# Kernel tuning notes

Hardware: AMD Instinct MI355X
Metric: run time of the kernel (lower is better)

The kernel has to match this reference:

```python
import jax, jax.numpy as jnp
import numpy as np

N_NODES = 200_000
N_EDGES = 6_400_000
N_GRAPHS = 512


def _graph_conv(x, src, dst, W_rel, b_rel, W_root, n_nodes):
    # PyG GraphConv (aggr='add'): lin_rel(sum_{j->i} x_j) + lin_root(x_i)
    agg = jax.ops.segment_sum(x[src], dst, num_segments=n_nodes)  # [N, in]
    return agg @ W_rel.T + b_rel + x @ W_root.T


def setup_inputs() -> dict:
    key = jax.random.key(0)
    ks = jax.random.split(key, 12)
    x = jax.random.normal(ks[0], (N_NODES, 3), dtype=jnp.float32)
    edge_index = jax.random.randint(ks[1], (2, N_EDGES), 0, N_NODES, dtype=jnp.int64)
    batch = jnp.sort(jax.random.randint(ks[2], (N_NODES,), 0, N_GRAPHS, dtype=jnp.int64))

    def xavier(k, shape):
        fan_out, fan_in = shape
        lim = np.sqrt(6.0 / (fan_in + fan_out)).astype(np.float32)
        return jax.random.uniform(k, shape, jnp.float32, -lim, lim)

    return {
        "x": x, "edge_index": edge_index, "batch": batch,
        "W1_rel": xavier(ks[3], (32, 3)),  "b1": jnp.zeros((32,), jnp.float32), "W1_root": xavier(ks[4], (32, 3)),
        "W2_rel": xavier(ks[5], (16, 32)), "b2": jnp.zeros((16,), jnp.float32), "W2_root": xavier(ks[6], (16, 32)),
        "W3_rel": xavier(ks[7], (8, 16)),  "b3": jnp.zeros((8,), jnp.float32),  "W3_root": xavier(ks[8], (8, 16)),
        "W_lin": xavier(ks[9], (1, 8)),    "b_lin": jnp.zeros((1,), jnp.float32),
    }


def reference(x, edge_index, batch,
              W1_rel, b1, W1_root,
              W2_rel, b2, W2_root,
              W3_rel, b3, W3_root,
              W_lin, b_lin):
    src, dst = edge_index[0], edge_index[1]
    h = jax.nn.relu(_graph_conv(x, src, dst, W1_rel, b1, W1_root, N_NODES))
    h = jax.nn.relu(_graph_conv(h, src, dst, W2_rel, b2, W2_root, N_NODES))
    h = jax.nn.relu(_graph_conv(h, src, dst, W3_rel, b3, W3_root, N_NODES))
    pooled = jax.ops.segment_max(h, batch, num_segments=N_GRAPHS)  # [G, 8]
    out = pooled @ W_lin.T + b_lin  # [G, 1]
    return out[:, 0]
```

## Files before the change

### kernel.cpp

```cpp
#include <hip/hip_runtime.h>
#include <hip/hip_fp16.h>

#define N_NODES 200000
#define N_EDGES 6400000
#define N_GRAPHS 512
#define HALFN 100000

#define NB1 196
#define CB 1024
#define NSB 16
#define NFB (NB1 * NSB)
#define CHUNK 4096
#define NCH 1563
#define NGRP 25
#define CPG 63
#define SCAP 3072
#define NBLK32 (N_NODES / 32)

typedef float vf4 __attribute__((ext_vector_type(4)));
typedef float vf2 __attribute__((ext_vector_type(2)));
typedef unsigned vu2 __attribute__((ext_vector_type(2)));

__device__ __forceinline__ unsigned ntload_u(const unsigned* p) {
  return __builtin_nontemporal_load(p);
}
__device__ __forceinline__ int ntload_i(const int* p) { return __builtin_nontemporal_load(p); }
__device__ __forceinline__ float ntload_f(const float* p) {
  return __builtin_nontemporal_load(p);
}
__device__ __forceinline__ void ntstore_u(unsigned* p, unsigned v) {
  __builtin_nontemporal_store(v, p);
}

__global__ __launch_bounds__(256) void count_kernel(const int* __restrict__ dst,
                                                    unsigned short* __restrict__ H) {
  __shared__ unsigned hist[4][NB1];
  int t = threadIdx.x, w = t >> 6;
  for (int i = t; i < 4 * NB1; i += 256) ((unsigned*)hist)[i] = 0;
  __syncthreads();
  int c = blockIdx.x;
  long e0 = (long)c * CHUNK;
  long rem = (long)N_EDGES - e0;
  int n = rem > CHUNK ? CHUNK : (int)rem;
  for (int i = t; i < n; i += 256) atomicAdd(&hist[w][dst[e0 + i] >> 10], 1u);
  __syncthreads();
  for (int b = t; b < NB1; b += 256)
    H[(size_t)c * NB1 + b] =
        (unsigned short)(hist[0][b] + hist[1][b] + hist[2][b] + hist[3][b]);
}

__global__ __launch_bounds__(256) void scan_bins1_kernel(unsigned short* __restrict__ H,
                                                         unsigned* __restrict__ P) {
  int b = blockIdx.x * 256 + threadIdx.x;
  int g = blockIdx.y;
  if (b >= NB1) return;
  int c0 = g * CPG, c1 = min(NCH, (g + 1) * CPG);
  unsigned run = 0;
  for (int c = c0; c < c1; c++) {
    unsigned t = H[(size_t)c * NB1 + b];
    H[(size_t)c * NB1 + b] = (unsigned short)run;
    run += t;
  }
  P[(size_t)g * NB1 + b] = run;
}

__global__ __launch_bounds__(256) void scan_bins2_kernel(unsigned* __restrict__ P,
                                                         unsigned* __restrict__ bucketTotal) {
  int b = blockIdx.x * 256 + threadIdx.x;
  if (b >= NB1) return;
  unsigned run = 0;
  for (int g = 0; g < NGRP; g++) {
    unsigned t = P[(size_t)g * NB1 + b];
    P[(size_t)g * NB1 + b] = run;
    run += t;
  }
  bucketTotal[b] = run;
}

__global__ __launch_bounds__(256) void scan_total_kernel(const unsigned* __restrict__ bucketTotal,
                                                         unsigned* __restrict__ bucketStart) {
  __shared__ unsigned partial[256];
  int t = threadIdx.x;
  unsigned v = (t < NB1) ? bucketTotal[t] : 0u;
  partial[t] = v;
  __syncthreads();
  for (int off = 1; off < 256; off <<= 1) {
    unsigned add = (t >= off) ? partial[t - off] : 0u;
    __syncthreads();
    partial[t] += add;
    __syncthreads();
  }
  if (t < NB1) bucketStart[t] = partial[t] - v;
  if (t == 0) bucketStart[NB1] = N_EDGES;
}

__global__ __launch_bounds__(256) void scatterA_kernel(
    const int* __restrict__ src, const int* __restrict__ dst,
    const unsigned short* __restrict__ H, const unsigned* __restrict__ P,
    const unsigned* __restrict__ bucketStart, unsigned* __restrict__ X1) {
  __shared__ unsigned ssort[CHUNK];
  __shared__ unsigned char sbort[CHUNK];
  __shared__ unsigned histw[4][NB1];
  __shared__ unsigned curw[4][NB1];
  __shared__ unsigned gbase[NB1];
  __shared__ unsigned partial[256];
  int t = threadIdx.x, w = t >> 6;
  int c = blockIdx.x;
  int g = c / CPG;
  long e0 = (long)c * CHUNK;
  long rem = (long)N_EDGES - e0;
  int n = rem > CHUNK ? CHUNK : (int)rem;
  for (int i = t; i < 4 * NB1; i += 256) ((unsigned*)histw)[i] = 0;
  __syncthreads();
  for (int i = t; i < n; i += 256) atomicAdd(&histw[w][dst[e0 + i] >> 10], 1u);
  __syncthreads();
  unsigned tot = 0, h0 = 0, h1 = 0, h2 = 0, h3 = 0;
  if (t < NB1) {
    h0 = histw[0][t]; h1 = histw[1][t]; h2 = histw[2][t]; h3 = histw[3][t];
    tot = h0 + h1 + h2 + h3;
  }
  partial[t] = tot;
  __syncthreads();
  for (int off = 1; off < 256; off <<= 1) {
    unsigned add = (t >= off) ? partial[t - off] : 0u;
    __syncthreads();
    partial[t] += add;
    __syncthreads();
  }
  if (t < NB1) {
    unsigned ex = partial[t] - tot;
    unsigned r = ex;
    curw[0][t] = r; r += h0;
    curw[1][t] = r; r += h1;
    curw[2][t] = r; r += h2;
    curw[3][t] = r;
    gbase[t] = bucketStart[t] + P[(size_t)g * NB1 + t] + (unsigned)H[(size_t)c * NB1 + t] - ex;
  }
  __syncthreads();
  for (int i = t; i < n; i += 256) {
    int d = dst[e0 + i], s = src[e0 + i];
    int b = d >> 10;
    unsigned r = atomicAdd(&curw[w][b], 1u);
    ssort[r] = ((unsigned)s << 10) | (unsigned)(d & 1023);
    sbort[r] = (unsigned char)b;
  }
  __syncthreads();
  for (int j = t; j < n; j += 256) X1[gbase[sbort[j]] + j] = ssort[j];
}

__global__ __launch_bounds__(1024) void scatterB_kernel(
    const unsigned* __restrict__ X1, const unsigned* __restrict__ bucketStart,
    unsigned* __restrict__ X2, unsigned* __restrict__ fineStart) {
  __shared__ unsigned histw[16][NSB];
  __shared__ unsigned binstart[NSB + 1];
  __shared__ unsigned cur[NSB];
  int t = threadIdx.x, w = t >> 6, b = blockIdx.x;
  unsigned cs0 = bucketStart[b], cs1 = bucketStart[b + 1];
  int n = (int)(cs1 - cs0);
  if (t < 16 * NSB) ((unsigned*)histw)[t] = 0;
  __syncthreads();
  for (int i = t; i < n; i += 1024)
    atomicAdd(&histw[w][(X1[cs0 + i] >> 6) & 15u], 1u);
  __syncthreads();
  if (t == 0) {
    unsigned run = 0;
    for (int k = 0; k < NSB; k++) {
      binstart[k] = run;
      unsigned tot = 0;
      for (int ww = 0; ww < 16; ww++) tot += histw[ww][k];
      run += tot;
    }
    binstart[NSB] = run;
  }
  __syncthreads();
  if (t < NSB) {
    fineStart[b * NSB + t] = cs0 + binstart[t];
    cur[t] = binstart[t];
  }
  if (b == NB1 - 1 && t == 0) fineStart[NFB] = cs1;
  __syncthreads();
  for (int i = t; i < n; i += 1024) {
    unsigned v = X1[cs0 + i];
    unsigned pos = atomicAdd(&cur[(v >> 6) & 15u], 1u);
    X2[cs0 + pos] = v;
  }
}

__global__ __launch_bounds__(256) void sort2_kernel(const unsigned* __restrict__ X2,
                                                    const unsigned* __restrict__ fineStart,
                                                    unsigned* __restrict__ packedB,
                                                    unsigned* __restrict__ nodeStart,
                                                    unsigned char* __restrict__ deltaSplit) {
  __shared__ unsigned buf[SCAP];
  __shared__ unsigned buf2[SCAP];
  __shared__ unsigned hist[128], base[128], cur[128];
  int t = threadIdx.x, b = blockIdx.x;
  unsigned s0 = fineStart[b], s1 = fineStart[b + 1];
  int n = (int)(s1 - s0);
  if (t < 128) hist[t] = 0;
  for (int i = t; i < n; i += 256) buf[i] = ntload_u(&X2[s0 + i]);
  __syncthreads();
  for (int i = t; i < n; i += 256) {
    unsigned v = buf[i];
    unsigned bin = ((v & 63u) << 1) | ((v >> 10) >= HALFN ? 1u : 0u);
    atomicAdd(&hist[bin], 1u);
  }
  __syncthreads();
  if (t == 0) {
    unsigned run = 0;
    for (int k = 0; k < 128; k++) {
      unsigned v = hist[k];
      base[k] = run;
      cur[k] = run;
      run += v;
    }
  }
  __syncthreads();
  if (t < 64) {
    int gn = b * 64 + t;
    if (gn <= N_NODES) nodeStart[gn] = s0 + base[2 * t];
    if (gn < N_NODES) deltaSplit[gn] = (unsigned char)(base[2 * t + 1] - base[2 * t]);
  }
  for (int i = t; i < n; i += 256) {
    unsigned v = buf[i];
    unsigned bin = ((v & 63u) << 1) | ((v >> 10) >= HALFN ? 1u : 0u);
    unsigned pos = atomicAdd(&cur[bin], 1u);
    buf2[pos] = v >> 10;
  }
  __syncthreads();
  for (int i = t; i < n; i += 256) ntstore_u(&packedB[s0 + i], buf2[i]);
}

__global__ __launch_bounds__(256) void xpad_kernel(const float* __restrict__ x,
                                                   uint2* __restrict__ xph) {
  int n = blockIdx.x * 256 + threadIdx.x;
  if (n >= N_NODES) return;
  __half2 a = __floats2half2_rn(x[3 * n], x[3 * n + 1]);
  __half2 b = __floats2half2_rn(x[3 * n + 2], 0.f);
  xph[n] = make_uint2(*(unsigned*)&a, *(unsigned*)&b);
}

__device__ __forceinline__ void half8_unpack(uint4 g, float* f) {
  const __half2* h2 = reinterpret_cast<const __half2*>(&g);
#pragma unroll
  for (int j = 0; j < 4; j++) {
    float2 fj = __half22float2(h2[j]);
    f[2 * j] = fj.x;
    f[2 * j + 1] = fj.y;
  }
}

__global__ __launch_bounds__(256) void layer1a_kernel(
    const unsigned* __restrict__ packed, const unsigned* __restrict__ nodeStart,
    const uint2* __restrict__ xph, float* __restrict__ agg) {
  __shared__ float plds[256 * 9];
  int t = threadIdx.x, ln = t >> 3, p = t & 7;
  int node = blockIdx.x * 32 + ln;
  unsigned s1v = ntload_u(&nodeStart[node + 1]);
  float a0 = 0.f, a1 = 0.f, a2 = 0.f;
  for (unsigned base = ntload_u(&nodeStart[node]) + p; base < s1v; base += 32) {
    unsigned i1 = base + 8, i2 = base + 16, i3 = base + 24;
    unsigned e0 = ntload_u(&packed[base]);
    unsigned e1 = ntload_u(&packed[i1]);
    unsigned e2 = ntload_u(&packed[i2]);
    unsigned e3 = ntload_u(&packed[i3]);
    uint2 g0 = xph[e0], g1 = xph[e1], g2 = xph[e2], g3 = xph[e3];
    float m1 = (i1 < s1v) ? 1.f : 0.f;
    float m2 = (i2 < s1v) ? 1.f : 0.f;
    float m3 = (i3 < s1v) ? 1.f : 0.f;
    float2 xy0 = __half22float2(*(const __half2*)&g0.x);
    float2 zw0 = __half22float2(*(const __half2*)&g0.y);
    float2 xy1 = __half22float2(*(const __half2*)&g1.x);
    float2 zw1 = __half22float2(*(const __half2*)&g1.y);
    float2 xy2 = __half22float2(*(const __half2*)&g2.x);
    float2 zw2 = __half22float2(*(const __half2*)&g2.y);
    float2 xy3 = __half22float2(*(const __half2*)&g3.x);
    float2 zw3 = __half22float2(*(const __half2*)&g3.y);
    a0 += xy0.x + m1 * xy1.x + m2 * xy2.x + m3 * xy3.x;
    a1 += xy0.y + m1 * xy1.y + m2 * xy2.y + m3 * xy3.y;
    a2 += zw0.x + m1 * zw1.x + m2 * zw2.x + m3 * zw3.x;
  }
  plds[t * 9] = a0; plds[t * 9 + 1] = a1; plds[t * 9 + 2] = a2;
  __syncthreads();
  if (p < 4) {
    int q0 = ln * 72 + p;
    float v = 0.f;
    if (p < 3)
      v = plds[q0] + plds[q0 + 9] + plds[q0 + 18] + plds[q0 + 27] +
          plds[q0 + 36] + plds[q0 + 45] + plds[q0 + 54] + plds[q0 + 63];
    agg[(size_t)node * 4 + p] = v;
  }
}

__global__ __launch_bounds__(256) void layer1b_kernel(
    const float* __restrict__ x, const float4* __restrict__ agg,
    const float* __restrict__ W1_rel, const float* __restrict__ b1,
    const float* __restrict__ W1_root,
    const float* __restrict__ W2_rel, const float* __restrict__ W2_root,
    uint4* __restrict__ t2h4, uint4* __restrict__ r2h4) {
  __shared__ float sW1rel[96], sW1root[96], sb1[32], sW2rel[512], sW2root[512];
  for (int i = threadIdx.x; i < 96; i += 256) { sW1rel[i] = W1_rel[i]; sW1root[i] = W1_root[i]; }
  for (int i = threadIdx.x; i < 32; i += 256) sb1[i] = b1[i];
  for (int i = threadIdx.x; i < 512; i += 256) { sW2rel[i] = W2_rel[i]; sW2root[i] = W2_root[i]; }
  __syncthreads();
  int node = blockIdx.x * 256 + threadIdx.x;
  if (node >= N_NODES) return;
  float4 A = agg[node];
  float xv0 = x[3 * node], xv1 = x[3 * node + 1], xv2 = x[3 * node + 2];
  float h[32];
#pragma unroll
  for (int k = 0; k < 32; k++) {
    float v = sW1rel[3 * k] * A.x + sW1rel[3 * k + 1] * A.y + sW1rel[3 * k + 2] * A.z +
              sW1root[3 * k] * xv0 + sW1root[3 * k + 1] * xv1 + sW1root[3 * k + 2] * xv2 +
              sb1[k];
    h[k] = fmaxf(v, 0.f);
  }
  unsigned tp[8];
#pragma unroll
  for (int j = 0; j < 16; j += 2) {
    float t0 = 0.f, t1 = 0.f;
#pragma unroll
    for (int k = 0; k < 32; k++) {
      t0 += sW2rel[32 * j + k] * h[k];
      t1 += sW2rel[32 * (j + 1) + k] * h[k];
    }
    __half2 pk = __halves2half2(__float2half_rn(t0), __float2half_rn(t1));
    tp[j >> 1] = *(unsigned*)&pk;
  }
  t2h4[(size_t)node * 2] = make_uint4(tp[0], tp[1], tp[2], tp[3]);
  t2h4[(size_t)node * 2 + 1] = make_uint4(tp[4], tp[5], tp[6], tp[7]);
  unsigned rp[8];
#pragma unroll
  for (int j = 0; j < 16; j += 2) {
    float r0 = 0.f, r1 = 0.f;
#pragma unroll
    for (int k = 0; k < 32; k++) {
      r0 += sW2root[32 * j + k] * h[k];
      r1 += sW2root[32 * (j + 1) + k] * h[k];
    }
    __half2 pk = __halves2half2(__float2half_rn(r0), __float2half_rn(r1));
    rp[j >> 1] = *(unsigned*)&pk;
  }
  r2h4[(size_t)node * 2] = make_uint4(rp[0], rp[1], rp[2], rp[3]);
  r2h4[(size_t)node * 2 + 1] = make_uint4(rp[4], rp[5], rp[6], rp[7]);
}

__global__ __launch_bounds__(256) void layer2g_kernel(
    const unsigned* __restrict__ packed, const unsigned* __restrict__ nodeStart,
    const unsigned char* __restrict__ deltaSplit,
    const uint4* __restrict__ t2h4, __half* __restrict__ agg2, int pass) {
  __shared__ float plds[256 * 17];
  int t = threadIdx.x, ln = t >> 3, p = t & 7;
  int node = blockIdx.x * 32 + ln;
  unsigned s0n = ntload_u(&nodeStart[node]);
  unsigned s1n = ntload_u(&nodeStart[node + 1]);
  unsigned split = s0n + (unsigned)deltaSplit[node];
  unsigned lo = pass ? split : s0n;
  unsigned hi = pass ? s1n : split;
  float acc[16];
#pragma unroll
  for (int j = 0; j < 16; j++) acc[j] = 0.f;
  for (unsigned base = lo + p; base < hi; base += 16) {
    unsigned i1 = base + 8;
    unsigned e0 = ntload_u(&packed[base]);
    unsigned e1r = ntload_u(&packed[i1]);
    bool in1 = i1 < hi;
    unsigned e1 = in1 ? e1r : e0;
    uint4 g0a = t2h4[(size_t)e0 * 2], g0b = t2h4[(size_t)e0 * 2 + 1];
    uint4 g1a = t2h4[(size_t)e1 * 2], g1b = t2h4[(size_t)e1 * 2 + 1];
    float f0[16], f1[16];
    half8_unpack(g0a, f0);
    half8_unpack(g0b, f0 + 8);
    half8_unpack(g1a, f1);
    half8_unpack(g1b, f1 + 8);
    float m1 = in1 ? 1.f : 0.f;
#pragma unroll
    for (int j = 0; j < 16; j++) acc[j] += f0[j] + m1 * f1[j];
  }
#pragma unroll
  for (int j = 0; j < 16; j++) plds[t * 17 + j] = acc[j];
  __syncthreads();
  int qb = ln * 8 * 17;
  float s0 = 0.f, s1 = 0.f;
#pragma unroll
  for (int k = 0; k < 8; k++) {
    s0 += plds[qb + k * 17 + 2 * p];
    s1 += plds[qb + k * 17 + 2 * p + 1];
  }
  __half* dst = &agg2[(size_t)node * 16 + 2 * p];
  if (pass) {
    __half2 old = *(const __half2*)dst;
    float2 of = __half22float2(old);
    s0 += of.x;
    s1 += of.y;
  }
  *(__half2*)dst = __halves2half2(__float2half_rn(s0), __float2half_rn(s1));
}

__global__ __launch_bounds__(256) void layer2e_kernel(
    const uint4* agg2q, const uint4* __restrict__ r2h4,
    const float* __restrict__ b2, const float* __restrict__ W3_rel,
    const float* __restrict__ W3_root, uint4* __restrict__ t3h4, float4* r34) {
  __shared__ float sW3rel[128], sW3root[128], sb2[16];
  for (int i = threadIdx.x; i < 128; i += 256) { sW3rel[i] = W3_rel[i]; sW3root[i] = W3_root[i]; }
  if (threadIdx.x < 16) sb2[threadIdx.x] = b2[threadIdx.x];
  __syncthreads();
  int node = blockIdx.x * 256 + threadIdx.x;
  if (node >= N_NODES) return;
  uint4 ga = agg2q[(size_t)node * 2];
  uint4 gb = agg2q[(size_t)node * 2 + 1];
  float ag[16];
  half8_unpack(ga, ag);
  half8_unpack(gb, ag + 8);
  uint4 ra = r2h4[(size_t)node * 2];
  uint4 rb = r2h4[(size_t)node * 2 + 1];
  float rv2[16];
  half8_unpack(ra, rv2);
  half8_unpack(rb, rv2 + 8);
  float h[16];
#pragma unroll
  for (int k = 0; k < 16; k++) h[k] = fmaxf(ag[k] + rv2[k] + sb2[k], 0.f);
  unsigned tp[4];
#pragma unroll
  for (int j = 0; j < 8; j += 2) {
    float t0 = 0.f, t1 = 0.f;
#pragma unroll
    for (int k = 0; k < 16; k++) {
      t0 += sW3rel[16 * j + k] * h[k];
      t1 += sW3rel[16 * (j + 1) + k] * h[k];
    }
    __half2 pk = __halves2half2(__float2half_rn(t0), __float2half_rn(t1));
    tp[j >> 1] = *(unsigned*)&pk;
  }
  t3h4[node] = make_uint4(tp[0], tp[1], tp[2], tp[3]);
  float rv[8];
#pragma unroll
  for (int j = 0; j < 8; j++) {
    float a = 0.f;
#pragma unroll
    for (int k = 0; k < 16; k++) a += sW3root[16 * j + k] * h[k];
    rv[j] = a;
  }
  r34[(size_t)node * 2] = make_float4(rv[0], rv[1], rv[2], rv[3]);
  r34[(size_t)node * 2 + 1] = make_float4(rv[4], rv[5], rv[6], rv[7]);
}

__global__ __launch_bounds__(256) void layer3_kernel(
    const unsigned* __restrict__ packed, const unsigned* __restrict__ nodeStart,
    const uint4* __restrict__ t3h4, const float* __restrict__ r3,
    const float* __restrict__ b3,
    const int* __restrict__ batch, unsigned* __restrict__ pooled) {
  __shared__ float plds[256 * 9];
  __shared__ float sb3[8];
  __shared__ int sgid[32];
  if (threadIdx.x < 8) sb3[threadIdx.x] = b3[threadIdx.x];
  __syncthreads();
  int t = threadIdx.x, ln = t >> 3, p = t & 7;
  int node = blockIdx.x * 32 + ln;
  unsigned s1v = ntload_u(&nodeStart[node + 1]);
  float acc[8];
#pragma unroll
  for (int j = 0; j < 8; j++) acc[j] = 0.f;
  for (unsigned base = ntload_u(&nodeStart[node]) + p; base < s1v; base += 32) {
    unsigned i1 = base + 8, i2 = base + 16, i3 = base + 24;
    unsigned e0 = ntload_u(&packed[base]);
    unsigned e1 = ntload_u(&packed[i1]);
    unsigned e2 = ntload_u(&packed[i2]);
    unsigned e3 = ntload_u(&packed[i3]);
    uint4 g0 = t3h4[e0];
    uint4 g1 = t3h4[e1];
    uint4 g2 = t3h4[e2];
    uint4 g3 = t3h4[e3];
    float m1 = (i1 < s1v) ? 1.f : 0.f;
    float m2 = (i2 < s1v) ? 1.f : 0.f;
    float m3 = (i3 < s1v) ? 1.f : 0.f;
    float f0[8], f1[8], f2[8], f3[8];
    half8_unpack(g0, f0);
    half8_unpack(g1, f1);
    half8_unpack(g2, f2);
    half8_unpack(g3, f3);
#pragma unroll
    for (int j = 0; j < 8; j++)
      acc[j] += f0[j] + m1 * f1[j] + m2 * f2[j] + m3 * f3[j];
  }
#pragma unroll
  for (int j = 0; j < 8; j++) plds[t * 9 + j] = acc[j];
  __syncthreads();
  int gg = ntload_i(&batch[node]);
  int q0 = ln * 72 + p;
  float v = plds[q0] + plds[q0 + 9] + plds[q0 + 18] + plds[q0 + 27] +
            plds[q0 + 36] + plds[q0 + 45] + plds[q0 + 54] + plds[q0 + 63];
  float h = fmaxf(v + sb3[p] + ntload_f(&r3[(size_t)node * 8 + p]), 0.f);
  __syncthreads();
  plds[ln * 9 + p] = h;
  if (p == 0) sgid[ln] = gg;
  __syncthreads();
  if (t < 8) {
    int gcur = sgid[0];
    float m = plds[t];
    for (int l = 1; l < 32; l++) {
      int g2 = sgid[l];
      float hv = plds[l * 9 + t];
      if (g2 != gcur) {
        atomicMax(&pooled[8 * gcur + t], __float_as_uint(m));
        gcur = g2;
        m = hv;
      } else {
        m = fmaxf(m, hv);
      }
    }
    atomicMax(&pooled[8 * gcur + t], __float_as_uint(m));
  }
}

__global__ __launch_bounds__(256) void final_kernel(
    const unsigned* __restrict__ pooled, const float* __restrict__ W_lin,
    const float* __restrict__ b_lin, float* __restrict__ out) {
  int g = blockIdx.x * blockDim.x + threadIdx.x;
  if (g >= N_GRAPHS) return;
  float acc = b_lin[0];
#pragma unroll
  for (int f = 0; f < 8; f++) acc += __uint_as_float(pooled[8 * g + f]) * W_lin[f];
  out[g] = acc;
}

extern "C" void kernel_launch(void* const* d_in, const int* in_sizes, int n_in,
                              void* d_out, int out_size, void* d_ws, size_t ws_size,
                              hipStream_t stream) {
  const float* x = (const float*)d_in[0];
  const int* ei = (const int*)d_in[1];
  const int* src = ei;
  const int* dst = ei + N_EDGES;
  const int* batch = (const int*)d_in[2];
  const float* W1_rel = (const float*)d_in[3];
  const float* b1 = (const float*)d_in[4];
  const float* W1_root = (const float*)d_in[5];
  const float* W2_rel = (const float*)d_in[6];
  const float* b2 = (const float*)d_in[7];
  const float* W2_root = (const float*)d_in[8];
  const float* W3_rel = (const float*)d_in[9];
  const float* b3 = (const float*)d_in[10];
  const float* W3_root = (const float*)d_in[11];
  const float* W_lin = (const float*)d_in[12];
  const float* b_lin = (const float*)d_in[13];
  float* out = (float*)d_out;

  char* ws = (char*)d_ws;
  unsigned* X2 = (unsigned*)(ws + 0);
  uint4* r2h = (uint4*)(ws + 0);
  __half* agg2 = (__half*)(ws + 6400000);
  float* r3 = (float*)(ws + 6400000);
  unsigned* t3h = (unsigned*)(ws + 12800000);
  unsigned* t2h = (unsigned*)(ws + 16000000);
  unsigned* X1 = (unsigned*)(ws + 25600000);
  unsigned* packedB = (unsigned*)(ws + 25600000);
  unsigned short* H = (unsigned short*)(ws + 51200128);
  unsigned* P = (unsigned*)(ws + 51812824);
  unsigned* bucketTotal = (unsigned*)(ws + 51832424);
  unsigned* bucketStart = (unsigned*)(ws + 51833208);
  unsigned* fineStart = (unsigned*)(ws + 51833996);
  float* agg = (float*)(ws + 52000000);
  uint2* xpadh = (uint2*)(ws + 55300000);
  unsigned* pooled = (unsigned*)(ws + 57600128);
  unsigned char* deltaSplit = (unsigned char*)(ws + 57616512);
  unsigned* nodeStart = (unsigned*)(ws + 57954016);

  hipMemsetAsync(pooled, 0, N_GRAPHS * 8 * sizeof(unsigned), stream);
  hipMemsetAsync(packedB + N_EDGES, 0, 128, stream);

  xpad_kernel<<<(N_NODES + 255) / 256, 256, 0, stream>>>(x, xpadh);

  count_kernel<<<NCH, 256, 0, stream>>>(dst, H);
  scan_bins1_kernel<<<dim3((NB1 + 255) / 256, NGRP), 256, 0, stream>>>(H, P);
  scan_bins2_kernel<<<(NB1 + 255) / 256, 256, 0, stream>>>(P, bucketTotal);
  scan_total_kernel<<<1, 256, 0, stream>>>(bucketTotal, bucketStart);
  scatterA_kernel<<<NCH, 256, 0, stream>>>(src, dst, H, P, bucketStart, X1);
  scatterB_kernel<<<NB1, 1024, 0, stream>>>(X1, bucketStart, X2, fineStart);
  sort2_kernel<<<NFB, 256, 0, stream>>>(X2, fineStart, packedB, nodeStart, deltaSplit);

  layer1a_kernel<<<NBLK32, 256, 0, stream>>>(packedB, nodeStart, xpadh, agg);
  layer1b_kernel<<<(N_NODES + 255) / 256, 256, 0, stream>>>(
      x, (const float4*)agg, W1_rel, b1, W1_root, W2_rel, W2_root,
      (uint4*)t2h, r2h);

  layer2g_kernel<<<NBLK32, 256, 0, stream>>>(packedB, nodeStart, deltaSplit,
                                             (const uint4*)t2h, agg2, 0);
  layer2g_kernel<<<NBLK32, 256, 0, stream>>>(packedB, nodeStart, deltaSplit,
                                             (const uint4*)t2h, agg2, 1);
  layer2e_kernel<<<(N_NODES + 255) / 256, 256, 0, stream>>>(
      (const uint4*)agg2, (const uint4*)r2h, b2, W3_rel, W3_root,
      (uint4*)t3h, (float4*)r3);

  layer3_kernel<<<NBLK32, 256, 0, stream>>>(packedB, nodeStart, (const uint4*)t3h, r3, b3,
                                            batch, pooled);
  final_kernel<<<(N_GRAPHS + 255) / 256, 256, 0, stream>>>(pooled, W_lin, b_lin, out);
}
```

Before: 416.8 us.

## Fuse second-level scatter and fine sort into one per-bucket LDS sort kernel

Replaces the two-pass scatterB plus sort2 (which wrote an intermediate X2 array to global memory and launched 3136 small blocks) with a single kernel per coarse bucket. Each block builds a 2048-bin histogram of (node, half) keys in shared memory, scans it in parallel, emits nodeStart and deltaSplit, and counting-sorts the bucket's entries into a large LDS buffer before writing packedB. This removes one full global read/write pass over the edge list and a launch. In exchange, only 196 blocks run, with about 150KB of LDS each, so occupancy and parallelism drop and X1 is read twice. Output aliases input memory (X1 and packedB share the same offset), which stays safe only because each block reads its range before storing it.

```diff
diff --git a/kernel.cpp b/kernel.cpp
--- a/kernel.cpp
+++ b/kernel.cpp
@@ -8,13 +8,11 @@
 
 #define NB1 196
 #define CB 1024
-#define NSB 16
-#define NFB (NB1 * NSB)
 #define CHUNK 4096
 #define NCH 1563
 #define NGRP 25
 #define CPG 63
-#define SCAP 3072
+#define BCAP 34816
 #define NBLK32 (N_NODES / 32)
 
 typedef float vf4 __attribute__((ext_vector_type(4)));
@@ -148,87 +146,58 @@
   for (int j = t; j < n; j += 256) X1[gbase[sbort[j]] + j] = ssort[j];
 }
 
-__global__ __launch_bounds__(1024) void scatterB_kernel(
-    const unsigned* __restrict__ X1, const unsigned* __restrict__ bucketStart,
-    unsigned* __restrict__ X2, unsigned* __restrict__ fineStart) {
-  __shared__ unsigned histw[16][NSB];
-  __shared__ unsigned binstart[NSB + 1];
-  __shared__ unsigned cur[NSB];
-  int t = threadIdx.x, w = t >> 6, b = blockIdx.x;
+__global__ __launch_bounds__(512) void sortBC_kernel(
+    const unsigned* X1r, const unsigned* __restrict__ bucketStart,
+    unsigned* packedB, unsigned* __restrict__ nodeStart,
+    unsigned char* __restrict__ deltaSplit) {
+  __shared__ unsigned buf[BCAP];
+  __shared__ unsigned hist[2048];
+  __shared__ unsigned cur[2048];
+  __shared__ unsigned partial[512];
+  int t = threadIdx.x, b = blockIdx.x;
   unsigned cs0 = bucketStart[b], cs1 = bucketStart[b + 1];
   int n = (int)(cs1 - cs0);
-  if (t < 16 * NSB) ((unsigned*)histw)[t] = 0;
-  __syncthreads();
-  for (int i = t; i < n; i += 1024)
-    atomicAdd(&histw[w][(X1[cs0 + i] >> 6) & 15u], 1u);
-  __syncthreads();
-  if (t == 0) {
-    unsigned run = 0;
-    for (int k = 0; k < NSB; k++) {
-      binstart[k] = run;
-      unsigned tot = 0;
-      for (int ww = 0; ww < 16; ww++) tot += histw[ww][k];
-      run += tot;
+  for (int i = t; i < 2048; i += 512) hist[i] = 0;
+  __syncthreads();
+  for (int i = t; i < n; i += 512) {
+    unsigned v = ntload_u(&X1r[cs0 + i]);
+    unsigned bin = ((v & 1023u) << 1) | ((v >> 10) >= HALFN ? 1u : 0u);
+    atomicAdd(&hist[bin], 1u);
+  }
+  __syncthreads();
+  unsigned a0 = hist[4 * t], a1 = hist[4 * t + 1], a2 = hist[4 * t + 2], a3 = hist[4 * t + 3];
+  unsigned sum = a0 + a1 + a2 + a3;
+  partial[t] = sum;
+  __syncthreads();
+  for (int off = 1; off < 512; off <<= 1) {
+    unsigned add = (t >= off) ? partial[t - off] : 0u;
+    __syncthreads();
+    partial[t] += add;
+    __syncthreads();
+  }
+  unsigned run = partial[t] - sum;
+  hist[4 * t] = run; cur[4 * t] = run; run += a0;
+  hist[4 * t + 1] = run; cur[4 * t + 1] = run; run += a1;
+  hist[4 * t + 2] = run; cur[4 * t + 2] = run; run += a2;
+  hist[4 * t + 3] = run; cur[4 * t + 3] = run;
+  __syncthreads();
+  for (int k = t; k < CB; k += 512) {
+    int gn = b * CB + k;
+    if (gn < N_NODES) {
+      nodeStart[gn] = cs0 + hist[2 * k];
+      deltaSplit[gn] = (unsigned char)(hist[2 * k + 1] - hist[2 * k]);
+    } else if (gn == N_NODES) {
+      nodeStart[gn] = cs0 + hist[2 * k];
     }
-    binstart[NSB] = run;
-  }
-  __syncthreads();
-  if (t < NSB) {
-    fineStart[b * NSB + t] = cs0 + binstart[t];
-    cur[t] = binstart[t];
-  }
-  if (b == NB1 - 1 && t == 0) fineStart[NFB] = cs1;
-  __syncthreads();
-  for (int i = t; i < n; i += 1024) {
-    unsigned v = X1[cs0 + i];
-    unsigned pos = atomicAdd(&cur[(v >> 6) & 15u], 1u);
-    X2[cs0 + pos] = v;
-  }
-}
-
-__global__ __launch_bounds__(256) void sort2_kernel(const unsigned* __restrict__ X2,
-                                                    const unsigned* __restrict__ fineStart,
-                                                    unsigned* __restrict__ packedB,
-                                                    unsigned* __restrict__ nodeStart,
-                                                    unsigned char* __restrict__ deltaSplit) {
-  __shared__ unsigned buf[SCAP];
-  __shared__ unsigned buf2[SCAP];
-  __shared__ unsigned hist[128], base[128], cur[128];
-  int t = threadIdx.x, b = blockIdx.x;
-  unsigned s0 = fineStart[b], s1 = fineStart[b + 1];
-  int n = (int)(s1 - s0);
-  if (t < 128) hist[t] = 0;
-  for (int i = t; i < n; i += 256) buf[i] = ntload_u(&X2[s0 + i]);
-  __syncthreads();
-  for (int i = t; i < n; i += 256) {
-    unsigned v = buf[i];
-    unsigned bin = ((v & 63u) << 1) | ((v >> 10) >= HALFN ? 1u : 0u);
-    atomicAdd(&hist[bin], 1u);
-  }
-  __syncthreads();
-  if (t == 0) {
-    unsigned run = 0;
-    for (int k = 0; k < 128; k++) {
-      unsigned v = hist[k];
-      base[k] = run;
-      cur[k] = run;
-      run += v;
-    }
-  }
-  __syncthreads();
-  if (t < 64) {
-    int gn = b * 64 + t;
-    if (gn <= N_NODES) nodeStart[gn] = s0 + base[2 * t];
-    if (gn < N_NODES) deltaSplit[gn] = (unsigned char)(base[2 * t + 1] - base[2 * t]);
-  }
-  for (int i = t; i < n; i += 256) {
-    unsigned v = buf[i];
-    unsigned bin = ((v & 63u) << 1) | ((v >> 10) >= HALFN ? 1u : 0u);
+  }
+  for (int i = t; i < n; i += 512) {
+    unsigned v = X1r[cs0 + i];
+    unsigned bin = ((v & 1023u) << 1) | ((v >> 10) >= HALFN ? 1u : 0u);
     unsigned pos = atomicAdd(&cur[bin], 1u);
-    buf2[pos] = v >> 10;
-  }
-  __syncthreads();
-  for (int i = t; i < n; i += 256) ntstore_u(&packedB[s0 + i], buf2[i]);
+    buf[pos] = v;
+  }
+  __syncthreads();
+  for (int i = t; i < n; i += 512) ntstore_u(&packedB[cs0 + i], buf[i] >> 10);
 }
 
 __global__ __launch_bounds__(256) void xpad_kernel(const float* __restrict__ x,
@@ -546,7 +515,6 @@
   float* out = (float*)d_out;
 
   char* ws = (char*)d_ws;
-  unsigned* X2 = (unsigned*)(ws + 0);
   uint4* r2h = (uint4*)(ws + 0);
   __half* agg2 = (__half*)(ws + 6400000);
   float* r3 = (float*)(ws + 6400000);
@@ -558,7 +526,6 @@
   unsigned* P = (unsigned*)(ws + 51812824);
   unsigned* bucketTotal = (unsigned*)(ws + 51832424);
   unsigned* bucketStart = (unsigned*)(ws + 51833208);
-  unsigned* fineStart = (unsigned*)(ws + 51833996);
   float* agg = (float*)(ws + 52000000);
   uint2* xpadh = (uint2*)(ws + 55300000);
   unsigned* pooled = (unsigned*)(ws + 57600128);
@@ -575,8 +542,7 @@
   scan_bins2_kernel<<<(NB1 + 255) / 256, 256, 0, stream>>>(P, bucketTotal);
   scan_total_kernel<<<1, 256, 0, stream>>>(bucketTotal, bucketStart);
   scatterA_kernel<<<NCH, 256, 0, stream>>>(src, dst, H, P, bucketStart, X1);
-  scatterB_kernel<<<NB1, 1024, 0, stream>>>(X1, bucketStart, X2, fineStart);
-  sort2_kernel<<<NFB, 256, 0, stream>>>(X2, fineStart, packedB, nodeStart, deltaSplit);
+  sortBC_kernel<<<NB1, 512, 0, stream>>>(X1, bucketStart, packedB, nodeStart, deltaSplit);
 
   layer1a_kernel<<<NBLK32, 256, 0, stream>>>(packedB, nodeStart, xpadh, agg);
   layer1b_kernel<<<(N_NODES + 255) / 256, 256, 0, stream>>>(
```

New measurement: 435.0 us. +4.4%, slower.
